# Kernel tuning notes

Measured on AMD Instinct MI355X. Metric: run time of the kernel, lower is better.

The kernel has to match this reference:

```python
import jax, jax.numpy as jnp
import numpy as np

DIM = 512
HEADS = 8
HEAD_DIM = DIM // HEADS


def setup_inputs() -> dict:
    key = jax.random.key(0)
    ks = jax.random.split(key, 8)
    B, T, C, H, W = 2, 8, DIM, 16, 16
    s = lambda fan: 1.0 / np.sqrt(fan)
    return {
        "features_seq": jax.random.normal(ks[0], (B, T, C, H, W), jnp.float32),
        # weights stored as [in, out] (math identical to torch Linear y = x @ W.T)
        "qkv_w": jax.random.normal(ks[1], (C, 3 * C), jnp.float32) * s(C),
        "qkv_b": jnp.zeros((3 * C,), jnp.float32),
        "proj_w": jax.random.normal(ks[2], (C, C), jnp.float32) * s(C),
        "proj_b": jnp.zeros((C,), jnp.float32),
        "ln1_g": jnp.ones((C,), jnp.float32),
        "ln1_b": jnp.zeros((C,), jnp.float32),
        "w1": jax.random.normal(ks[3], (C, 4 * C), jnp.float32) * s(C),
        "b1": jnp.zeros((4 * C,), jnp.float32),
        "w2": jax.random.normal(ks[4], (4 * C, C), jnp.float32) * s(4 * C),
        "b2": jnp.zeros((C,), jnp.float32),
        "ln2_g": jnp.ones((C,), jnp.float32),
        "ln2_b": jnp.zeros((C,), jnp.float32),
    }


def _layernorm(x, g, b, eps=1e-5):
    mu = jnp.mean(x, axis=-1, keepdims=True)
    var = jnp.var(x, axis=-1, keepdims=True)
    return (x - mu) * jax.lax.rsqrt(var + eps) * g + b


def _mhsa(x, qkv_w, qkv_b, proj_w, proj_b):
    B, N, C = x.shape
    qkv = (x @ qkv_w + qkv_b).reshape(B, N, 3, HEADS, HEAD_DIM)
    qkv = jnp.transpose(qkv, (2, 0, 3, 1, 4))  # [3, B, h, N, d]
    q, k, v = qkv[0], qkv[1], qkv[2]
    scale = HEAD_DIM ** -0.5
    attn = jnp.einsum("bhqd,bhkd->bhqk", q, k) * scale
    attn = jax.nn.softmax(attn, axis=-1)
    o = jnp.einsum("bhqk,bhkd->bhqd", attn, v)
    o = jnp.transpose(o, (0, 2, 1, 3)).reshape(B, N, C)
    return o @ proj_w + proj_b


def reference(features_seq, qkv_w, qkv_b, proj_w, proj_b, ln1_g, ln1_b,
              w1, b1, w2, b2, ln2_g, ln2_b):
    B, T, C, H, W = features_seq.shape
    L = H * W
    # [B,T,C,H,W] -> [B, T*L, C]
    x = features_seq.reshape(B, T, C, L).transpose(0, 1, 3, 2).reshape(B, T * L, C)
    x = x + _mhsa(_layernorm(x, ln1_g, ln1_b), qkv_w, qkv_b, proj_w, proj_b)
    h = _layernorm(x, ln2_g, ln2_b)
    h = jax.nn.gelu(h @ w1 + b1, approximate=False) @ w2 + b2
    x = x + h
    # back to [B, T, C, H, W]
    out = x.reshape(B, T, L, C).transpose(0, 1, 3, 2).reshape(B, T, C, H, W)
    return out
```

## Files before the change

kernel.cpp:

```cpp
#include <hip/hip_runtime.h>
#include <stdint.h>
#include <math.h>

typedef __attribute__((ext_vector_type(8))) short short8;
typedef __attribute__((ext_vector_type(4))) float f32x4;

__device__ __forceinline__ ushort f2bf(float f) {
    union { float f; uint32_t i; } v; v.f = f;
    uint32_t r = v.i + 0x7FFFu + ((v.i >> 16) & 1u);
    return (ushort)(r >> 16);
}
__device__ __forceinline__ float bf2f(ushort u) {
    union { uint32_t i; float f; } v; v.i = ((uint32_t)u) << 16; return v.f;
}

__device__ __forceinline__ void gload_lds16(const ushort* gp, ushort* lp) {
    __builtin_amdgcn_global_load_lds(
        (const __attribute__((address_space(1))) void*)gp,
        (__attribute__((address_space(3))) void*)lp, 16, 0, 0);
}

__global__ __launch_bounds__(512) void prep_kernel(const float* __restrict__ in,
        const float* __restrict__ g, const float* __restrict__ bta,
        float* __restrict__ x, ushort* __restrict__ xln) {
    int token = blockIdx.x;
    int c = threadIdx.x;
    int b = token >> 11;
    int n = token & 2047;
    int t = n >> 8;
    int l = n & 255;
    size_t iidx = (((size_t)((b * 8 + t) * 512 + c)) << 8) + l;
    float v = in[iidx];
    x[(size_t)token * 512 + c] = v;

    float s = v, s2 = v * v;
    #pragma unroll
    for (int off = 32; off > 0; off >>= 1) {
        s  += __shfl_down(s, off, 64);
        s2 += __shfl_down(s2, off, 64);
    }
    __shared__ float ps[8], ps2[8];
    int wave = threadIdx.x >> 6, lane = threadIdx.x & 63;
    if (lane == 0) { ps[wave] = s; ps2[wave] = s2; }
    __syncthreads();
    float mu = 0.f, m2 = 0.f;
    #pragma unroll
    for (int i = 0; i < 8; i++) { mu += ps[i]; m2 += ps2[i]; }
    mu *= (1.0f / 512.0f); m2 *= (1.0f / 512.0f);
    float rs = rsqrtf(m2 - mu * mu + 1e-5f);
    float y = (v - mu) * rs * g[c] + bta[c];
    xln[(size_t)token * 512 + c] = f2bf(y);
}

__global__ __launch_bounds__(512) void ln2_kernel(const float* __restrict__ xin,
        const float* __restrict__ g, const float* __restrict__ bta,
        ushort* __restrict__ out) {
    int token = blockIdx.x;
    int c = threadIdx.x;
    float v = xin[(size_t)token * 512 + c];
    float s = v, s2 = v * v;
    #pragma unroll
    for (int off = 32; off > 0; off >>= 1) {
        s  += __shfl_down(s, off, 64);
        s2 += __shfl_down(s2, off, 64);
    }
    __shared__ float ps[8], ps2[8];
    int wave = threadIdx.x >> 6, lane = threadIdx.x & 63;
    if (lane == 0) { ps[wave] = s; ps2[wave] = s2; }
    __syncthreads();
    float mu = 0.f, m2 = 0.f;
    #pragma unroll
    for (int i = 0; i < 8; i++) { mu += ps[i]; m2 += ps2[i]; }
    mu *= (1.0f / 512.0f); m2 *= (1.0f / 512.0f);
    float rs = rsqrtf(m2 - mu * mu + 1e-5f);
    float y = (v - mu) * rs * g[c] + bta[c];
    out[(size_t)token * 512 + c] = f2bf(y);
}

__global__ __launch_bounds__(256) void wtrans_kernel(
        const float* __restrict__ wa, ushort* __restrict__ ta,
        const float* __restrict__ wb, ushort* __restrict__ tb,
        const float* __restrict__ wc, ushort* __restrict__ tc,
        const float* __restrict__ wd, ushort* __restrict__ td) {
    __shared__ float tile[32][33];
    int bid = blockIdx.x;
    const float* W; ushort* T; int K, N, tn, tk;
    if (bid < 768)       { W = wa; T = ta; K = 512;  N = 1536; tn = bid % 48; tk = bid / 48; }
    else if (bid < 1024) { bid -= 768;  W = wb; T = tb; K = 512;  N = 512;  tn = bid % 16; tk = bid / 16; }
    else if (bid < 2048) { bid -= 1024; W = wc; T = tc; K = 512;  N = 2048; tn = bid % 64; tk = bid / 64; }
    else                 { bid -= 2048; W = wd; T = td; K = 2048; N = 512;  tn = bid % 16; tk = bid / 16; }
    int n0 = tn * 32, k0 = tk * 32;
    int tx = threadIdx.x & 31, ty = threadIdx.x >> 5;
    #pragma unroll
    for (int i = 0; i < 4; i++)
        tile[ty + i * 8][tx] = W[(size_t)(k0 + ty + i * 8) * N + n0 + tx];
    __syncthreads();
    #pragma unroll
    for (int i = 0; i < 4; i++) {
        int nn = ty + i * 8;
        T[(size_t)(n0 + nn) * K + k0 + tx] = f2bf(tile[tx][nn]);
    }
}

#define EPI_BF16   0
#define EPI_F32RES 1
#define EPI_GELU   2

template<int EPI>
__global__ __launch_bounds__(256) void gemm_kernel(
        const ushort* __restrict__ A, const ushort* __restrict__ Bt,
        const float* __restrict__ bias, const float* __restrict__ resid,
        float* __restrict__ outF, ushort* __restrict__ outB,
        int M, int N, int K) {
    __shared__ __align__(16) ushort As[64 * 64];
    __shared__ __align__(16) ushort Bs[128 * 64];
    int tid = threadIdx.x;
    int wave = tid >> 6, lane = tid & 63;
    int l16 = lane & 15, quad = lane >> 4;
    int wc = wave;
    int m0 = blockIdx.y * 64, n0 = blockIdx.x * 128;

    f32x4 acc[4][2] = {};
    for (int k0 = 0; k0 < K; k0 += 64) {
        #pragma unroll
        for (int c = 0; c < 2; c++) {
            int e = c * 256 + tid;
            int row = e >> 3, ch = e & 7;
            int sc = ch ^ (row & 7);
            gload_lds16(A + (size_t)(m0 + row) * K + k0 + sc * 8,
                        As + (size_t)(c * 256 + wave * 64) * 8);
        }
        #pragma unroll
        for (int c = 0; c < 4; c++) {
            int e = c * 256 + tid;
            int row = e >> 3, ch = e & 7;
            int sc = ch ^ (row & 7);
            gload_lds16(Bt + (size_t)(n0 + row) * K + k0 + sc * 8,
                        Bs + (size_t)(c * 256 + wave * 64) * 8);
        }
        __syncthreads();
        #pragma unroll
        for (int kk = 0; kk < 2; kk++) {
            short8 af[4], bf[2];
            #pragma unroll
            for (int i = 0; i < 4; i++) {
                int row = i * 16 + l16;
                af[i] = *(const short8*)&As[row * 64 + (((kk * 4 + quad) ^ (row & 7)) * 8)];
            }
            #pragma unroll
            for (int j = 0; j < 2; j++) {
                int row = wc * 32 + j * 16 + l16;
                bf[j] = *(const short8*)&Bs[row * 64 + (((kk * 4 + quad) ^ (row & 7)) * 8)];
            }
            #pragma unroll
            for (int i = 0; i < 4; i++)
                #pragma unroll
                for (int j = 0; j < 2; j++)
                    acc[i][j] = __builtin_amdgcn_mfma_f32_16x16x32_bf16(af[i], bf[j], acc[i][j], 0, 0, 0);
        }
        __syncthreads();
    }
    #pragma unroll
    for (int i = 0; i < 4; i++) {
        int row_base = m0 + i * 16 + quad * 4;
        #pragma unroll
        for (int j = 0; j < 2; j++) {
            int col = n0 + wc * 32 + j * 16 + l16;
            float bvf = bias[col];
            #pragma unroll
            for (int r = 0; r < 4; r++) {
                int row = row_base + r;
                float v = acc[i][j][r] + bvf;
                if constexpr (EPI == EPI_F32RES) {
                    outF[(size_t)row * N + col] = v + resid[(size_t)row * N + col];
                } else if constexpr (EPI == EPI_GELU) {
                    float gg = 0.5f * v * (1.0f + erff(v * 0.70710678118654752f));
                    outB[(size_t)row * N + col] = f2bf(gg);
                } else {
                    outB[(size_t)row * N + col] = f2bf(v);
                }
            }
        }
    }
}

__global__ __launch_bounds__(512) void flash_kernel(const ushort* __restrict__ qkv,
        ushort* __restrict__ o) {
    __shared__ __align__(16) char smem[55424];
    auto Ks  = (ushort (*)[64][72])smem;
    auto Vt  = (ushort (*)[4640])(smem + 18432);
    auto Pt  = (ushort (*)[16][72])(smem + 36992);
    auto cbuf = (float (*)[24][64])smem;

    int tid = threadIdx.x;
    int wave = tid >> 6, lane = tid & 63;
    int kh = wave >> 2;
    int wq = wave & 3;
    int l16 = lane & 15, quad = lane >> 4;
    int bidx = blockIdx.x;
    int qt = bidx & 31;
    int h = (bidx >> 5) & 7;
    int b = bidx >> 8;
    int q0 = qt * 64;
    const size_t base = (size_t)b * 2048 * 1536;

    int htid = tid & 255;
    int srow = htid >> 2;
    int sg   = htid & 3;
    int sdb  = sg * 16;
    const ushort* kgbase = qkv + base + 512  + h * 64 + sdb;
    const ushort* vgbase = qkv + base + 1024 + h * 64 + sdb;
    int vldsoff = sdb * 72 + sg * 8 + srow;

    short8 aq[2];
    {
        int qrow = q0 + wq * 16 + l16;
        const ushort* qp = qkv + base + (size_t)qrow * 1536 + h * 64;
        aq[0] = *(const short8*)(qp + quad * 8);
        aq[1] = *(const short8*)(qp + 32 + quad * 8);
    }
    f32x4 accO[4] = {};
    float mrow[4] = {-INFINITY, -INFINITY, -INFINITY, -INFINITY};
    float lrow[4] = {0.f, 0.f, 0.f, 0.f};

    {
        int kb = kh * 1024;
        const ushort* kp = kgbase + (size_t)(kb + srow) * 1536;
        short8 k0 = *(const short8*)kp;
        short8 k1 = *(const short8*)(kp + 8);
        const ushort* vp = vgbase + (size_t)(kb + srow) * 1536;
        short8 v0 = *(const short8*)vp;
        short8 v1 = *(const short8*)(vp + 8);
        *(short8*)&Ks[kh][srow][sdb]     = k0;
        *(short8*)&Ks[kh][srow][sdb + 8] = k1;
        #pragma unroll
        for (int i = 0; i < 8; i++) Vt[kh][vldsoff + i * 72] = (ushort)v0[i];
        #pragma unroll
        for (int i = 0; i < 8; i++) Vt[kh][vldsoff + (8 + i) * 72] = (ushort)v1[i];
    }
    __syncthreads();

    for (int it = 0; it < 16; ++it) {
        short8 nk0, nk1, nv0, nv1;
        bool pre = (it < 15);
        if (pre) {
            int kb = kh * 1024 + (it + 1) * 64;
            const ushort* kp = kgbase + (size_t)(kb + srow) * 1536;
            nk0 = *(const short8*)kp;
            nk1 = *(const short8*)(kp + 8);
            const ushort* vp = vgbase + (size_t)(kb + srow) * 1536;
            nv0 = *(const short8*)vp;
            nv1 = *(const short8*)(vp + 8);
        }
        f32x4 sacc[4] = {};
        __builtin_amdgcn_s_setprio(1);
        #pragma unroll
        for (int c = 0; c < 2; c++) {
            #pragma unroll
            for (int s = 0; s < 4; s++) {
                short8 kf = *(short8*)&Ks[kh][s * 16 + l16][c * 32 + quad * 8];
                sacc[s] = __builtin_amdgcn_mfma_f32_16x16x32_bf16(aq[c], kf, sacc[s], 0, 0, 0);
            }
        }
        __builtin_amdgcn_s_setprio(0);
        float p[4][4];
        #pragma unroll
        for (int r = 0; r < 4; r++) {
            float tm = fmaxf(fmaxf(sacc[0][r], sacc[1][r]), fmaxf(sacc[2][r], sacc[3][r]));
            #pragma unroll
            for (int off = 1; off < 16; off <<= 1)
                tm = fmaxf(tm, __shfl_xor(tm, off, 16));
            float mn = fmaxf(mrow[r], tm * 0.125f);
            float al = __expf(mrow[r] - mn);
            float rsum = 0.f;
            #pragma unroll
            for (int s = 0; s < 4; s++) {
                float pv = __expf(sacc[s][r] * 0.125f - mn);
                p[s][r] = pv;
                rsum += pv;
            }
            #pragma unroll
            for (int off = 1; off < 16; off <<= 1)
                rsum += __shfl_xor(rsum, off, 16);
            lrow[r] = lrow[r] * al + rsum;
            mrow[r] = mn;
            #pragma unroll
            for (int s = 0; s < 4; s++) accO[s][r] *= al;
        }
        #pragma unroll
        for (int s = 0; s < 4; s++)
            #pragma unroll
            for (int r = 0; r < 4; r++)
                Pt[wave][quad * 4 + r][s * 16 + l16] = f2bf(p[s][r]);
        __builtin_amdgcn_s_setprio(1);
        #pragma unroll
        for (int ks = 0; ks < 2; ks++) {
            short8 ap = *(short8*)&Pt[wave][l16][ks * 32 + quad * 8];
            #pragma unroll
            for (int s = 0; s < 4; s++) {
                short8 vf = *(short8*)&Vt[kh][(s * 16 + l16) * 72 + s * 8 + ks * 32 + quad * 8];
                accO[s] = __builtin_amdgcn_mfma_f32_16x16x32_bf16(ap, vf, accO[s], 0, 0, 0);
            }
        }
        __builtin_amdgcn_s_setprio(0);
        __syncthreads();
        if (pre) {
            *(short8*)&Ks[kh][srow][sdb]     = nk0;
            *(short8*)&Ks[kh][srow][sdb + 8] = nk1;
            #pragma unroll
            for (int i = 0; i < 8; i++) Vt[kh][vldsoff + i * 72] = (ushort)nv0[i];
            #pragma unroll
            for (int i = 0; i < 8; i++) Vt[kh][vldsoff + (8 + i) * 72] = (ushort)nv1[i];
        }
        __syncthreads();
    }
    if (kh == 1) {
        #pragma unroll
        for (int r = 0; r < 4; r++) {
            cbuf[wq][r][lane]     = mrow[r];
            cbuf[wq][4 + r][lane] = lrow[r];
        }
        #pragma unroll
        for (int s = 0; s < 4; s++)
            #pragma unroll
            for (int r = 0; r < 4; r++)
                cbuf[wq][8 + s * 4 + r][lane] = accO[s][r];
    }
    __syncthreads();
    if (kh == 0) {
        #pragma unroll
        for (int r = 0; r < 4; r++) {
            float m1 = cbuf[wq][r][lane];
            float l1 = cbuf[wq][4 + r][lane];
            float mn = fmaxf(mrow[r], m1);
            float a0 = __expf(mrow[r] - mn);
            float a1 = __expf(m1 - mn);
            float rl = 1.0f / (lrow[r] * a0 + l1 * a1);
            int qrow = q0 + wq * 16 + quad * 4 + r;
            #pragma unroll
            for (int s = 0; s < 4; s++) {
                float ov = (accO[s][r] * a0 + cbuf[wq][8 + s * 4 + r][lane] * a1) * rl;
                o[((size_t)(b * 2048 + qrow)) * 512 + h * 64 + s * 16 + l16] = f2bf(ov);
            }
        }
    }
}

__global__ __launch_bounds__(256) void tout_kernel(const float* __restrict__ x3,
        float* __restrict__ out) {
    __shared__ float tile[32][33];
    int bt = blockIdx.z;
    int l0 = blockIdx.y * 32;
    int c0 = blockIdx.x * 32;
    int tx = threadIdx.x, ty = threadIdx.y;
    #pragma unroll
    for (int i = 0; i < 4; i++) {
        int l = ty + i * 8;
        tile[l][tx] = x3[((size_t)bt * 256 + l0 + l) * 512 + c0 + tx];
    }
    __syncthreads();
    #pragma unroll
    for (int i = 0; i < 4; i++) {
        int cc = ty + i * 8;
        out[((size_t)bt * 512 + c0 + cc) * 256 + l0 + tx] = tile[tx][cc];
    }
}

extern "C" void kernel_launch(void* const* d_in, const int* in_sizes, int n_in,
                              void* d_out, int out_size, void* d_ws, size_t ws_size,
                              hipStream_t stream) {
    const float* in_feat = (const float*)d_in[0];
    const float* qkv_w  = (const float*)d_in[1];
    const float* qkv_b  = (const float*)d_in[2];
    const float* proj_w = (const float*)d_in[3];
    const float* proj_b = (const float*)d_in[4];
    const float* ln1_g  = (const float*)d_in[5];
    const float* ln1_b  = (const float*)d_in[6];
    const float* w1     = (const float*)d_in[7];
    const float* b1     = (const float*)d_in[8];
    const float* w2     = (const float*)d_in[9];
    const float* b2     = (const float*)d_in[10];
    const float* ln2_g  = (const float*)d_in[11];
    const float* ln2_b  = (const float*)d_in[12];

    char* ws = (char*)d_ws;
    float*  x    = (float*) (ws);
    float*  x2   = (float*) (ws + 8388608);
    ushort* xln  = (ushort*)(ws + 16777216);
    ushort* h2   = (ushort*)(ws + 20971520);
    ushort* ao   = (ushort*)(ws + 25165824);
    ushort* qkv  = (ushort*)(ws + 29360128);
    ushort* gbuf = (ushort*)(ws + 41943040);

    char* scr = (char*)d_out;
    ushort* qkvT = (ushort*)(scr);
    ushort* projT = (ushort*)(scr + 1572864);
    ushort* w1T  = (ushort*)(scr + 2097152);
    ushort* w2T  = (ushort*)(scr + 4194304);

    wtrans_kernel<<<3072, 256, 0, stream>>>(qkv_w, qkvT, proj_w, projT,
                                            w1, w1T, w2, w2T);
    prep_kernel<<<4096, 512, 0, stream>>>(in_feat, ln1_g, ln1_b, x, xln);
    gemm_kernel<EPI_BF16><<<dim3(12, 64), 256, 0, stream>>>(
        xln, qkvT, qkv_b, nullptr, nullptr, qkv, 4096, 1536, 512);
    flash_kernel<<<512, 512, 0, stream>>>(qkv, ao);
    gemm_kernel<EPI_F32RES><<<dim3(4, 64), 256, 0, stream>>>(
        ao, projT, proj_b, x, x2, nullptr, 4096, 512, 512);
    ln2_kernel<<<4096, 512, 0, stream>>>(x2, ln2_g, ln2_b, h2);
    gemm_kernel<EPI_GELU><<<dim3(16, 64), 256, 0, stream>>>(
        h2, w1T, b1, nullptr, nullptr, gbuf, 4096, 2048, 512);
    gemm_kernel<EPI_F32RES><<<dim3(4, 64), 256, 0, stream>>>(
        gbuf, w2T, b2, x2, x, nullptr, 4096, 512, 2048);
    tout_kernel<<<dim3(16, 8, 16), dim3(32, 8), 0, stream>>>(x, (float*)d_out);
}
```

Before: 254.2 us.

## Double-buffer GEMM LDS tiles and transpose flash-attention score layout

The GEMM kernel now double-buffers its A/B tiles in LDS, issuing the next tile's global-to-LDS loads before the current tile's MFMAs. This overlaps memory with compute and cuts one barrier per K step, at the cost of twice the LDS. The flash kernel swaps the MFMA operands so each lane holds one query row. Row max and sum then need only two cross-lane shuffles, P is written as vectorized 4-element stores to a smaller LDS buffer in two halves, and the output is stored as 4-wide vectors, with LDS reduced to allow more resident blocks.

```diff
diff --git a/kernel.cpp b/kernel.cpp
--- a/kernel.cpp
+++ b/kernel.cpp
@@ -4,6 +4,7 @@
 
 typedef __attribute__((ext_vector_type(8))) short short8;
 typedef __attribute__((ext_vector_type(4))) float f32x4;
+typedef __attribute__((ext_vector_type(4))) ushort ushort4v;
 
 __device__ __forceinline__ ushort f2bf(float f) {
     union { float f; uint32_t i; } v; v.f = f;
@@ -112,23 +113,24 @@
         const float* __restrict__ bias, const float* __restrict__ resid,
         float* __restrict__ outF, ushort* __restrict__ outB,
         int M, int N, int K) {
-    __shared__ __align__(16) ushort As[64 * 64];
-    __shared__ __align__(16) ushort Bs[128 * 64];
+    __shared__ __align__(16) ushort As[2][64 * 64];
+    __shared__ __align__(16) ushort Bs[2][128 * 64];
     int tid = threadIdx.x;
     int wave = tid >> 6, lane = tid & 63;
     int l16 = lane & 15, quad = lane >> 4;
     int wc = wave;
     int m0 = blockIdx.y * 64, n0 = blockIdx.x * 128;
 
-    f32x4 acc[4][2] = {};
-    for (int k0 = 0; k0 < K; k0 += 64) {
+    auto stage = [&](int bufi, int k0) {
+        ushort* Ab = &As[bufi][0];
+        ushort* Bb = &Bs[bufi][0];
         #pragma unroll
         for (int c = 0; c < 2; c++) {
             int e = c * 256 + tid;
             int row = e >> 3, ch = e & 7;
             int sc = ch ^ (row & 7);
             gload_lds16(A + (size_t)(m0 + row) * K + k0 + sc * 8,
-                        As + (size_t)(c * 256 + wave * 64) * 8);
+                        Ab + (size_t)(c * 256 + wave * 64) * 8);
         }
         #pragma unroll
         for (int c = 0; c < 4; c++) {
@@ -136,29 +138,42 @@
             int row = e >> 3, ch = e & 7;
             int sc = ch ^ (row & 7);
             gload_lds16(Bt + (size_t)(n0 + row) * K + k0 + sc * 8,
-                        Bs + (size_t)(c * 256 + wave * 64) * 8);
-        }
-        __syncthreads();
+                        Bb + (size_t)(c * 256 + wave * 64) * 8);
+        }
+    };
+
+    f32x4 acc[4][2] = {};
+    stage(0, 0);
+    asm volatile("s_waitcnt vmcnt(0)" ::: "memory");
+    __builtin_amdgcn_s_barrier();
+    __builtin_amdgcn_sched_barrier(0);
+    int nt = K >> 6;
+    for (int t = 0; t < nt; ++t) {
+        int cur = t & 1;
+        if (t + 1 < nt) stage(cur ^ 1, (t + 1) << 6);
+        const ushort* Ac = &As[cur][0];
+        const ushort* Bc = &Bs[cur][0];
         #pragma unroll
         for (int kk = 0; kk < 2; kk++) {
             short8 af[4], bf[2];
-            #pragma unroll
-            for (int i = 0; i < 4; i++) {
-                int row = i * 16 + l16;
-                af[i] = *(const short8*)&As[row * 64 + (((kk * 4 + quad) ^ (row & 7)) * 8)];
-            }
-            #pragma unroll
-            for (int j = 0; j < 2; j++) {
-                int row = wc * 32 + j * 16 + l16;
-                bf[j] = *(const short8*)&Bs[row * 64 + (((kk * 4 + quad) ^ (row & 7)) * 8)];
-            }
+            int slot = ((kk * 4 + quad) ^ (l16 & 7)) * 8;
+            #pragma unroll
+            for (int i = 0; i < 4; i++)
+                af[i] = *(const short8*)&Ac[(i * 16 + l16) * 64 + slot];
+            #pragma unroll
+            for (int j = 0; j < 2; j++)
+                bf[j] = *(const short8*)&Bc[(wc * 32 + j * 16 + l16) * 64 + slot];
             #pragma unroll
             for (int i = 0; i < 4; i++)
                 #pragma unroll
                 for (int j = 0; j < 2; j++)
                     acc[i][j] = __builtin_amdgcn_mfma_f32_16x16x32_bf16(af[i], bf[j], acc[i][j], 0, 0, 0);
         }
-        __syncthreads();
+        if (t + 1 < nt) {
+            asm volatile("s_waitcnt vmcnt(0)" ::: "memory");
+            __builtin_amdgcn_s_barrier();
+            __builtin_amdgcn_sched_barrier(0);
+        }
     }
     #pragma unroll
     for (int i = 0; i < 4; i++) {
@@ -184,13 +199,13 @@
     }
 }
 
-__global__ __launch_bounds__(512) void flash_kernel(const ushort* __restrict__ qkv,
+__global__ __launch_bounds__(512, 6) void flash_kernel(const ushort* __restrict__ qkv,
         ushort* __restrict__ o) {
-    __shared__ __align__(16) char smem[55424];
+    __shared__ __align__(16) char smem[47232];
     auto Ks  = (ushort (*)[64][72])smem;
     auto Vt  = (ushort (*)[4640])(smem + 18432);
-    auto Pt  = (ushort (*)[16][72])(smem + 36992);
-    auto cbuf = (float (*)[24][64])smem;
+    auto Pt  = (ushort (*)[16][40])(smem + 36992);
+    auto cbuf = (float (*)[18][64])smem;
 
     int tid = threadIdx.x;
     int wave = tid >> 6, lane = tid & 63;
@@ -220,8 +235,7 @@
         aq[1] = *(const short8*)(qp + 32 + quad * 8);
     }
     f32x4 accO[4] = {};
-    float mrow[4] = {-INFINITY, -INFINITY, -INFINITY, -INFINITY};
-    float lrow[4] = {0.f, 0.f, 0.f, 0.f};
+    float mrow = -INFINITY, lrow = 0.f;
 
     {
         int kb = kh * 1024;
@@ -259,50 +273,61 @@
             #pragma unroll
             for (int s = 0; s < 4; s++) {
                 short8 kf = *(short8*)&Ks[kh][s * 16 + l16][c * 32 + quad * 8];
-                sacc[s] = __builtin_amdgcn_mfma_f32_16x16x32_bf16(aq[c], kf, sacc[s], 0, 0, 0);
+                sacc[s] = __builtin_amdgcn_mfma_f32_16x16x32_bf16(kf, aq[c], sacc[s], 0, 0, 0);
             }
         }
         __builtin_amdgcn_s_setprio(0);
-        float p[4][4];
-        #pragma unroll
-        for (int r = 0; r < 4; r++) {
-            float tm = fmaxf(fmaxf(sacc[0][r], sacc[1][r]), fmaxf(sacc[2][r], sacc[3][r]));
-            #pragma unroll
-            for (int off = 1; off < 16; off <<= 1)
-                tm = fmaxf(tm, __shfl_xor(tm, off, 16));
-            float mn = fmaxf(mrow[r], tm * 0.125f);
-            float al = __expf(mrow[r] - mn);
-            float rsum = 0.f;
+        float tm = sacc[0][0];
+        #pragma unroll
+        for (int s = 0; s < 4; s++)
+            #pragma unroll
+            for (int r = 0; r < 4; r++) tm = fmaxf(tm, sacc[s][r]);
+        tm = fmaxf(tm, __shfl_xor(tm, 16, 64));
+        tm = fmaxf(tm, __shfl_xor(tm, 32, 64));
+        float mn = fmaxf(mrow, tm * 0.125f);
+        float al = __expf(mrow - mn);
+        float rsum = 0.f;
+        ushort4v w4[4];
+        #pragma unroll
+        for (int s = 0; s < 4; s++)
+            #pragma unroll
+            for (int r = 0; r < 4; r++) {
+                float pv = __expf(sacc[s][r] * 0.125f - mn);
+                rsum += pv;
+                w4[s][r] = f2bf(pv);
+            }
+        rsum += __shfl_xor(rsum, 16, 64);
+        rsum += __shfl_xor(rsum, 32, 64);
+        lrow = lrow * al + rsum;
+        mrow = mn;
+        #pragma unroll
+        for (int s = 0; s < 4; s++)
+            #pragma unroll
+            for (int r = 0; r < 4; r++) accO[s][r] *= al;
+        *(ushort4v*)&Pt[wave][l16][quad * 4]      = w4[0];
+        *(ushort4v*)&Pt[wave][l16][16 + quad * 4] = w4[1];
+        {
+            short8 ap = *(short8*)&Pt[wave][l16][quad * 8];
+            __builtin_amdgcn_s_setprio(1);
             #pragma unroll
             for (int s = 0; s < 4; s++) {
-                float pv = __expf(sacc[s][r] * 0.125f - mn);
-                p[s][r] = pv;
-                rsum += pv;
-            }
-            #pragma unroll
-            for (int off = 1; off < 16; off <<= 1)
-                rsum += __shfl_xor(rsum, off, 16);
-            lrow[r] = lrow[r] * al + rsum;
-            mrow[r] = mn;
-            #pragma unroll
-            for (int s = 0; s < 4; s++) accO[s][r] *= al;
-        }
-        #pragma unroll
-        for (int s = 0; s < 4; s++)
-            #pragma unroll
-            for (int r = 0; r < 4; r++)
-                Pt[wave][quad * 4 + r][s * 16 + l16] = f2bf(p[s][r]);
-        __builtin_amdgcn_s_setprio(1);
-        #pragma unroll
-        for (int ks = 0; ks < 2; ks++) {
-            short8 ap = *(short8*)&Pt[wave][l16][ks * 32 + quad * 8];
+                short8 vf = *(short8*)&Vt[kh][(s * 16 + l16) * 72 + s * 8 + quad * 8];
+                accO[s] = __builtin_amdgcn_mfma_f32_16x16x32_bf16(vf, ap, accO[s], 0, 0, 0);
+            }
+            __builtin_amdgcn_s_setprio(0);
+        }
+        *(ushort4v*)&Pt[wave][l16][quad * 4]      = w4[2];
+        *(ushort4v*)&Pt[wave][l16][16 + quad * 4] = w4[3];
+        {
+            short8 ap = *(short8*)&Pt[wave][l16][quad * 8];
+            __builtin_amdgcn_s_setprio(1);
             #pragma unroll
             for (int s = 0; s < 4; s++) {
-                short8 vf = *(short8*)&Vt[kh][(s * 16 + l16) * 72 + s * 8 + ks * 32 + quad * 8];
-                accO[s] = __builtin_amdgcn_mfma_f32_16x16x32_bf16(ap, vf, accO[s], 0, 0, 0);
-            }
-        }
-        __builtin_amdgcn_s_setprio(0);
+                short8 vf = *(short8*)&Vt[kh][(s * 16 + l16) * 72 + s * 8 + 32 + quad * 8];
+                accO[s] = __builtin_amdgcn_mfma_f32_16x16x32_bf16(vf, ap, accO[s], 0, 0, 0);
+            }
+            __builtin_amdgcn_s_setprio(0);
+        }
         __syncthreads();
         if (pre) {
             *(short8*)&Ks[kh][srow][sdb]     = nk0;
@@ -315,33 +340,32 @@
         __syncthreads();
     }
     if (kh == 1) {
-        #pragma unroll
-        for (int r = 0; r < 4; r++) {
-            cbuf[wq][r][lane]     = mrow[r];
-            cbuf[wq][4 + r][lane] = lrow[r];
-        }
+        cbuf[wq][0][lane] = mrow;
+        cbuf[wq][1][lane] = lrow;
         #pragma unroll
         for (int s = 0; s < 4; s++)
             #pragma unroll
             for (int r = 0; r < 4; r++)
-                cbuf[wq][8 + s * 4 + r][lane] = accO[s][r];
+                cbuf[wq][2 + s * 4 + r][lane] = accO[s][r];
     }
     __syncthreads();
     if (kh == 0) {
-        #pragma unroll
-        for (int r = 0; r < 4; r++) {
-            float m1 = cbuf[wq][r][lane];
-            float l1 = cbuf[wq][4 + r][lane];
-            float mn = fmaxf(mrow[r], m1);
-            float a0 = __expf(mrow[r] - mn);
-            float a1 = __expf(m1 - mn);
-            float rl = 1.0f / (lrow[r] * a0 + l1 * a1);
-            int qrow = q0 + wq * 16 + quad * 4 + r;
-            #pragma unroll
-            for (int s = 0; s < 4; s++) {
-                float ov = (accO[s][r] * a0 + cbuf[wq][8 + s * 4 + r][lane] * a1) * rl;
-                o[((size_t)(b * 2048 + qrow)) * 512 + h * 64 + s * 16 + l16] = f2bf(ov);
-            }
+        float m1 = cbuf[wq][0][lane];
+        float l1 = cbuf[wq][1][lane];
+        float mn = fmaxf(mrow, m1);
+        float a0 = __expf(mrow - mn);
+        float a1 = __expf(m1 - mn);
+        float rl = 1.0f / (lrow * a0 + l1 * a1);
+        int qrow = q0 + wq * 16 + l16;
+        #pragma unroll
+        for (int s = 0; s < 4; s++) {
+            ushort4v ov4;
+            #pragma unroll
+            for (int r = 0; r < 4; r++) {
+                float ov = (accO[s][r] * a0 + cbuf[wq][2 + s * 4 + r][lane] * a1) * rl;
+                ov4[r] = f2bf(ov);
+            }
+            *(ushort4v*)&o[((size_t)(b * 2048 + qrow)) * 512 + h * 64 + s * 16 + quad * 4] = ov4;
         }
     }
 }
```

Result: faster. 242.6 us (-4.6%).
